# Kernel tuning notes

Hardware: AMD Instinct MI355X
Metric: run time of the kernel (lower is better)

Reference implementation:

```python
import jax, jax.numpy as jnp
import numpy as np

TOPK = 2
NUM_BODY_POINTS = 17
HIDDEN = 64


def bilinear_grid_sample(feat, grid):
    """F.grid_sample(feat, grid, mode='bilinear', padding_mode='zeros', align_corners=False).
    feat: [B,C,H,W]; grid: [B,L,K,2] in [-1,1], grid[...,0]=x (width), grid[...,1]=y (height).
    Returns [B,C,L,K]."""
    B, C, H, W = feat.shape
    x = (grid[..., 0] + 1.0) * (0.5 * W) - 0.5  # [B,L,K]
    y = (grid[..., 1] + 1.0) * (0.5 * H) - 0.5
    x0 = jnp.floor(x)
    y0 = jnp.floor(y)
    wx1 = x - x0
    wy1 = y - y0
    featf = feat.reshape(B, C, H * W)

    def gather(xi, yi):
        valid = (xi >= 0) & (xi < W) & (yi >= 0) & (yi < H)  # [B,L,K]
        xc = jnp.clip(xi, 0, W - 1).astype(jnp.int32)
        yc = jnp.clip(yi, 0, H - 1).astype(jnp.int32)
        idx = (yc * W + xc).reshape(B, -1)  # [B, L*K]
        v = jax.vmap(lambda f, i: f[:, i])(featf, idx)  # [B,C,L*K]
        v = v.reshape(B, C, *xi.shape[1:])  # [B,C,L,K]
        return v * valid[:, None].astype(feat.dtype)

    w00 = ((1 - wx1) * (1 - wy1))[:, None]
    w10 = (wx1 * (1 - wy1))[:, None]
    w01 = ((1 - wx1) * wy1)[:, None]
    w11 = (wx1 * wy1)[:, None]
    return (gather(x0, y0) * w00 + gather(x0 + 1, y0) * w10
            + gather(x0, y0 + 1) * w01 + gather(x0 + 1, y0 + 1) * w11)


def setup_inputs() -> dict:
    key = jax.random.key(0)
    ks = jax.random.split(key, 8)
    B, L, K, C, H, Wd = 16, 1000, NUM_BODY_POINTS, 17, 256, 256
    in_dim = K * (TOPK + 1)
    scores = jax.random.normal(ks[0], (B, L, 1), dtype=jnp.float32)
    pred_poses = jax.random.uniform(ks[1], (B, L, 2 * K), dtype=jnp.float32)
    feat = jax.random.normal(ks[2], (B, C, H, Wd), dtype=jnp.float32)
    s1 = 1.0 / np.sqrt(in_dim)
    s2 = 1.0 / np.sqrt(HIDDEN)
    w1 = jax.random.uniform(ks[3], (HIDDEN, in_dim), minval=-s1, maxval=s1, dtype=jnp.float32)
    b1 = jax.random.uniform(ks[4], (HIDDEN,), minval=-s1, maxval=s1, dtype=jnp.float32)
    w2 = jax.random.uniform(ks[5], (1, HIDDEN), minval=-s2, maxval=s2, dtype=jnp.float32)
    b2 = jax.random.uniform(ks[6], (1,), minval=-s2, maxval=s2, dtype=jnp.float32)
    return {"scores": scores, "pred_poses": pred_poses, "feat": feat,
            "w1": w1, "b1": b1, "w2": w2, "b2": b2}


def reference(scores, pred_poses, feat, w1, b1, w2, b2):
    B, L = pred_poses.shape[:2]
    poses = pred_poses.reshape(B, L, NUM_BODY_POINTS, 2)
    sampled = bilinear_grid_sample(feat, 2.0 * poses - 1.0)  # [B,C,L,K]
    sampled = jnp.transpose(sampled, (0, 2, 3, 1))  # [B,L,K,C]
    prob_topk, _ = jax.lax.top_k(sampled, TOPK)  # [B,L,K,topk]
    stat = jnp.concatenate([prob_topk, prob_topk.mean(axis=-1, keepdims=True)], axis=-1)
    x = stat.reshape(B, L, -1)  # [B,L,K*(topk+1)]
    h = jax.nn.relu(jnp.einsum('bli,hi->blh', x, w1) + b1)
    quality = jnp.einsum('blh,oh->blo', h, w2) + b2  # [B,L,1]
    return scores + quality
```

## Files before the change

kernel.cpp:

```cpp
#include <hip/hip_runtime.h>
#include <hip/hip_bf16.h>
#include <math.h>

#define NB 16
#define NL 1000
#define NK 17
#define NC 17
#define NH 256
#define NW 256
#define HID 64
#define IN_DIM 51
#define NPAIR (NB*NL)
#define PADC 20
#define STATW 52
#define NSAMP (NPAIR*NK)
#define SAMP_PER_XCD (NSAMP/8)
#define BLKS_B 133
#define PPB_C 32
#define PPB_F 15

#define TOP2(v) do { const float _v = (v); \
    if (_v > m1) { m2 = m1; m1 = _v; } else if (_v > m2) { m2 = _v; } } while (0)

__global__ __launch_bounds__(256) void transpose_feat(
    const float* __restrict__ feat, float* __restrict__ featT)
{
    __shared__ float s[NC][257];
    const int bid = blockIdx.x;
    const int l   = ((bid & 7) << 9) | (bid >> 3);
    const int b   = l >> 8;
    const int hw0 = (l & 255) << 8;
    const int tid = threadIdx.x;
    const float* fb = feat + (size_t)b * NC * (NH * NW) + hw0;
    #pragma unroll
    for (int c = 0; c < NC; ++c)
        s[c][tid] = fb[c * (NH * NW) + tid];
    __syncthreads();
    float4* outp = reinterpret_cast<float4*>(
        featT + ((size_t)b * (NH * NW) + hw0) * PADC);
    #pragma unroll
    for (int i = tid; i < 256 * PADC / 4; i += 256) {
        const int p = i / 5;
        const int j = i - 5 * p;
        float4 v;
        if (j < 4) {
            const int c = 4 * j;
            v = make_float4(s[c][p], s[c + 1][p], s[c + 2][p], s[c + 3][p]);
        } else {
            v = make_float4(s[16][p], 0.f, 0.f, 0.f);
        }
        outp[i] = v;
    }
}

__global__ __launch_bounds__(256) void sample_top2(
    const float* __restrict__ pred_poses,
    const float* __restrict__ featT,
    float* __restrict__ stat)
{
    const int xcd = blockIdx.x & 7;
    const int idx = blockIdx.x >> 3;
    const int sl  = idx * 256 + threadIdx.x;
    if (sl >= SAMP_PER_XCD) return;
    const int s    = xcd * SAMP_PER_XCD + sl;
    const int pair = s / NK;
    const int k    = s - pair * NK;
    const int b    = pair / NL;

    const float2 p = *reinterpret_cast<const float2*>(
        pred_poses + (size_t)pair * (2 * NK) + 2 * k);
    const float gx = 2.0f * p.x - 1.0f;
    const float gy = 2.0f * p.y - 1.0f;
    const float fx = (gx + 1.0f) * (0.5f * NW) - 0.5f;
    const float fy = (gy + 1.0f) * (0.5f * NH) - 0.5f;
    const float x0f = floorf(fx), y0f = floorf(fy);
    const float wx = fx - x0f,   wy = fy - y0f;
    const int ix0 = (int)x0f, iy0 = (int)y0f;
    const int ix1 = ix0 + 1,  iy1 = iy0 + 1;
    const float vx0 = (ix0 >= 0 && ix0 < NW) ? 1.f : 0.f;
    const float vx1 = (ix1 >= 0 && ix1 < NW) ? 1.f : 0.f;
    const float vy0 = (iy0 >= 0 && iy0 < NH) ? 1.f : 0.f;
    const float vy1 = (iy1 >= 0 && iy1 < NH) ? 1.f : 0.f;
    const float w00 = (1.f - wx) * (1.f - wy) * vx0 * vy0;
    const float w10 = wx * (1.f - wy) * vx1 * vy0;
    const float w01 = (1.f - wx) * wy * vx0 * vy1;
    const float w11 = wx * wy * vx1 * vy1;
    const int cx0 = min(max(ix0, 0), NW - 1), cx1 = min(max(ix1, 0), NW - 1);
    const int cy0 = min(max(iy0, 0), NH - 1), cy1 = min(max(iy1, 0), NH - 1);
    const float* fb  = featT + (size_t)b * (NH * NW) * PADC;
    const float* p00 = fb + (size_t)(cy0 * NW + cx0) * PADC;
    const float* p10 = fb + (size_t)(cy0 * NW + cx1) * PADC;
    const float* p01 = fb + (size_t)(cy1 * NW + cx0) * PADC;
    const float* p11 = fb + (size_t)(cy1 * NW + cx1) * PADC;

    float m1 = -INFINITY, m2 = -INFINITY;
    #pragma unroll
    for (int j = 0; j < 4; ++j) {
        const float4 a  = *reinterpret_cast<const float4*>(p00 + 4 * j);
        const float4 bq = *reinterpret_cast<const float4*>(p10 + 4 * j);
        const float4 c  = *reinterpret_cast<const float4*>(p01 + 4 * j);
        const float4 d  = *reinterpret_cast<const float4*>(p11 + 4 * j);
        TOP2(w00 * a.x + w10 * bq.x + w01 * c.x + w11 * d.x);
        TOP2(w00 * a.y + w10 * bq.y + w01 * c.y + w11 * d.y);
        TOP2(w00 * a.z + w10 * bq.z + w01 * c.z + w11 * d.z);
        TOP2(w00 * a.w + w10 * bq.w + w01 * c.w + w11 * d.w);
    }
    TOP2(w00 * p00[16] + w10 * p10[16] + w01 * p01[16] + w11 * p11[16]);

    float* sp = stat + (size_t)pair * STATW + 3 * k;
    sp[0] = m1;
    sp[1] = m2;
    sp[2] = 0.5f * (m1 + m2);
}

__global__ __launch_bounds__(256) void mlp_head(
    const float* __restrict__ scores,
    const float* __restrict__ stat,
    const float* __restrict__ w1,
    const float* __restrict__ b1,
    const float* __restrict__ w2,
    const float* __restrict__ b2,
    float* __restrict__ out)
{
    __shared__ float s_w1[HID * IN_DIM];
    __shared__ float s_b1[HID];
    __shared__ float s_w2[HID];
    const int tid = threadIdx.x;
    for (int i = tid; i < HID * IN_DIM; i += 256) s_w1[i] = w1[i];
    if (tid < HID) { s_b1[tid] = b1[tid]; s_w2[tid] = w2[tid]; }
    __syncthreads();

    const int lane = tid & 63;
    const int wv   = tid >> 6;
    float w1r[IN_DIM];
    #pragma unroll
    for (int i = 0; i < IN_DIM; ++i) w1r[i] = s_w1[lane * IN_DIM + i];
    const float hb = s_b1[lane];
    const float hw = s_w2[lane];
    const float vb2 = b2[0];

    const int p0 = blockIdx.x * PPB_C + wv * (PPB_C / 4);
    #pragma unroll
    for (int j = 0; j < PPB_C / 4; ++j) {
        const int pair = p0 + j;
        const float* xp = stat + (size_t)pair * STATW;
        float h = hb;
        #pragma unroll
        for (int i = 0; i < IN_DIM; ++i)
            h = fmaf(xp[i], w1r[i], h);
        h = fmaxf(h, 0.f);
        float pval = h * hw;
        #pragma unroll
        for (int off = 32; off >= 1; off >>= 1)
            pval += __shfl_xor(pval, off, 64);
        if (lane == 0) out[pair] = scores[pair] + pval + vb2;
    }
}

__global__ __launch_bounds__(256) void lqe_fused_direct(
    const float* __restrict__ scores,
    const float* __restrict__ pred_poses,
    const float* __restrict__ feat,
    const float* __restrict__ w1,
    const float* __restrict__ b1,
    const float* __restrict__ w2,
    const float* __restrict__ b2,
    float* __restrict__ out)
{
    __shared__ float s_w1[HID * IN_DIM];
    __shared__ float s_b1[HID];
    __shared__ float s_w2[HID];
    __shared__ float s_x[PPB_F][IN_DIM + 1];

    const int tid = threadIdx.x;
    for (int i = tid; i < HID * IN_DIM; i += 256) s_w1[i] = w1[i];
    if (tid < HID) { s_b1[tid] = b1[tid]; s_w2[tid] = w2[tid]; }

    if (tid < PPB_F * NK) {
        const int lp = tid / NK;
        const int k  = tid - lp * NK;
        const int pair = blockIdx.x * PPB_F + lp;
        if (pair < NPAIR) {
            const int b = pair / NL;
            const float2 p = *reinterpret_cast<const float2*>(
                pred_poses + (size_t)pair * (2 * NK) + 2 * k);
            const float gx = 2.0f * p.x - 1.0f;
            const float gy = 2.0f * p.y - 1.0f;
            const float fx = (gx + 1.0f) * (0.5f * NW) - 0.5f;
            const float fy = (gy + 1.0f) * (0.5f * NH) - 0.5f;
            const float x0f = floorf(fx), y0f = floorf(fy);
            const float wx = fx - x0f,   wy = fy - y0f;
            const int ix0 = (int)x0f, iy0 = (int)y0f;
            const int ix1 = ix0 + 1,  iy1 = iy0 + 1;
            const float vx0 = (ix0 >= 0 && ix0 < NW) ? 1.f : 0.f;
            const float vx1 = (ix1 >= 0 && ix1 < NW) ? 1.f : 0.f;
            const float vy0 = (iy0 >= 0 && iy0 < NH) ? 1.f : 0.f;
            const float vy1 = (iy1 >= 0 && iy1 < NH) ? 1.f : 0.f;
            const float w00 = (1.f - wx) * (1.f - wy) * vx0 * vy0;
            const float w10 = wx * (1.f - wy) * vx1 * vy0;
            const float w01 = (1.f - wx) * wy * vx0 * vy1;
            const float w11 = wx * wy * vx1 * vy1;
            const int cx0 = min(max(ix0, 0), NW - 1), cx1 = min(max(ix1, 0), NW - 1);
            const int cy0 = min(max(iy0, 0), NH - 1), cy1 = min(max(iy1, 0), NH - 1);
            const int o00 = cy0 * NW + cx0, o10 = cy0 * NW + cx1;
            const int o01 = cy1 * NW + cx0, o11 = cy1 * NW + cx1;
            const float* fb = feat + (size_t)b * NC * NH * NW;
            float m1 = -INFINITY, m2 = -INFINITY;
            #pragma unroll
            for (int c = 0; c < NC; ++c) {
                const float* fc = fb + c * (NH * NW);
                TOP2(w00 * fc[o00] + w10 * fc[o10] + w01 * fc[o01] + w11 * fc[o11]);
            }
            s_x[lp][3 * k + 0] = m1;
            s_x[lp][3 * k + 1] = m2;
            s_x[lp][3 * k + 2] = 0.5f * (m1 + m2);
        }
    }
    __syncthreads();

    const int wv = tid >> 6;
    const int lane = tid & 63;
    const float vb2 = b2[0];
    for (int lp = wv; lp < PPB_F; lp += 4) {
        const int pair = blockIdx.x * PPB_F + lp;
        if (pair >= NPAIR) break;
        float h = s_b1[lane];
        #pragma unroll
        for (int i = 0; i < IN_DIM; ++i)
            h = fmaf(s_x[lp][i], s_w1[lane * IN_DIM + i], h);
        h = fmaxf(h, 0.f);
        float pval = h * s_w2[lane];
        #pragma unroll
        for (int off = 32; off >= 1; off >>= 1)
            pval += __shfl_xor(pval, off, 64);
        if (lane == 0) out[pair] = scores[pair] + pval + vb2;
    }
}

extern "C" void kernel_launch(void* const* d_in, const int* in_sizes, int n_in,
                              void* d_out, int out_size, void* d_ws, size_t ws_size,
                              hipStream_t stream) {
    const float* scores     = (const float*)d_in[0];
    const float* pred_poses = (const float*)d_in[1];
    const float* feat       = (const float*)d_in[2];
    const float* w1         = (const float*)d_in[3];
    const float* b1         = (const float*)d_in[4];
    const float* w2         = (const float*)d_in[5];
    const float* b2         = (const float*)d_in[6];
    float* out = (float*)d_out;

    const size_t bytesT = (size_t)NB * NH * NW * PADC * sizeof(float);
    const size_t bytesS = (size_t)NPAIR * STATW * sizeof(float);

    if (ws_size >= bytesT + bytesS) {
        float* featT = (float*)d_ws;
        float* stat  = (float*)((char*)d_ws + bytesT);
        transpose_feat<<<NB * 256, 256, 0, stream>>>(feat, featT);
        sample_top2<<<8 * BLKS_B, 256, 0, stream>>>(pred_poses, featT, stat);
        mlp_head<<<NPAIR / PPB_C, 256, 0, stream>>>(scores, stat,
                                                    w1, b1, w2, b2, out);
    } else {
        const int grid = (NPAIR + PPB_F - 1) / PPB_F;
        lqe_fused_direct<<<grid, 256, 0, stream>>>(scores, pred_poses, feat,
                                                   w1, b1, w2, b2, out);
    }
}
```

Before: 179.2 us.

## Split each bilinear sample across four lanes, one per corner, with shuffle reduction

```diff
diff --git a/kernel.cpp b/kernel.cpp
--- a/kernel.cpp
+++ b/kernel.cpp
@@ -14,10 +14,10 @@
 #define PADC 20
 #define STATW 52
 #define NSAMP (NPAIR*NK)
-#define SAMP_PER_XCD (NSAMP/8)
-#define BLKS_B 133
 #define PPB_C 32
 #define PPB_F 15
+
+typedef float f32x4 __attribute__((ext_vector_type(4)));
 
 #define TOP2(v) do { const float _v = (v); \
     if (_v > m1) { m2 = m1; m1 = _v; } else if (_v > m2) { m2 = _v; } } while (0)
@@ -58,11 +58,9 @@
     const float* __restrict__ featT,
     float* __restrict__ stat)
 {
-    const int xcd = blockIdx.x & 7;
-    const int idx = blockIdx.x >> 3;
-    const int sl  = idx * 256 + threadIdx.x;
-    if (sl >= SAMP_PER_XCD) return;
-    const int s    = xcd * SAMP_PER_XCD + sl;
+    const int t  = blockIdx.x * 256 + threadIdx.x;
+    const int s  = t >> 2;
+    const int cr = t & 3;
     const int pair = s / NK;
     const int k    = s - pair * NK;
     const int b    = pair / NL;
@@ -75,42 +73,53 @@
     const float fy = (gy + 1.0f) * (0.5f * NH) - 0.5f;
     const float x0f = floorf(fx), y0f = floorf(fy);
     const float wx = fx - x0f,   wy = fy - y0f;
-    const int ix0 = (int)x0f, iy0 = (int)y0f;
-    const int ix1 = ix0 + 1,  iy1 = iy0 + 1;
-    const float vx0 = (ix0 >= 0 && ix0 < NW) ? 1.f : 0.f;
-    const float vx1 = (ix1 >= 0 && ix1 < NW) ? 1.f : 0.f;
-    const float vy0 = (iy0 >= 0 && iy0 < NH) ? 1.f : 0.f;
-    const float vy1 = (iy1 >= 0 && iy1 < NH) ? 1.f : 0.f;
-    const float w00 = (1.f - wx) * (1.f - wy) * vx0 * vy0;
-    const float w10 = wx * (1.f - wy) * vx1 * vy0;
-    const float w01 = (1.f - wx) * wy * vx0 * vy1;
-    const float w11 = wx * wy * vx1 * vy1;
-    const int cx0 = min(max(ix0, 0), NW - 1), cx1 = min(max(ix1, 0), NW - 1);
-    const int cy0 = min(max(iy0, 0), NH - 1), cy1 = min(max(iy1, 0), NH - 1);
-    const float* fb  = featT + (size_t)b * (NH * NW) * PADC;
-    const float* p00 = fb + (size_t)(cy0 * NW + cx0) * PADC;
-    const float* p10 = fb + (size_t)(cy0 * NW + cx1) * PADC;
-    const float* p01 = fb + (size_t)(cy1 * NW + cx0) * PADC;
-    const float* p11 = fb + (size_t)(cy1 * NW + cx1) * PADC;
-
+
+    const int dx = cr & 1, dy = cr >> 1;
+    const int ix = (int)x0f + dx;
+    const int iy = (int)y0f + dy;
+    const float fxw = dx ? wx : (1.f - wx);
+    const float fyw = dy ? wy : (1.f - wy);
+    const float vx  = (ix >= 0 && ix < NW) ? 1.f : 0.f;
+    const float vy  = (iy >= 0 && iy < NH) ? 1.f : 0.f;
+    const float wc  = fxw * fyw * vx * vy;
+    const int cx = min(max(ix, 0), NW - 1);
+    const int cy = min(max(iy, 0), NH - 1);
+    const float* rp = featT + ((size_t)b * (NH * NW) + (size_t)(cy * NW + cx)) * PADC;
+
+    const f32x4 r0 = __builtin_nontemporal_load((const f32x4*)(rp));
+    const f32x4 r1 = __builtin_nontemporal_load((const f32x4*)(rp + 4));
+    const f32x4 r2 = __builtin_nontemporal_load((const f32x4*)(rp + 8));
+    const f32x4 r3 = __builtin_nontemporal_load((const f32x4*)(rp + 12));
+    const float r4 = __builtin_nontemporal_load(rp + 16);
+
+    float v[NC];
+    #pragma unroll
+    for (int j = 0; j < 4; ++j) {
+        v[4 * j + 0] = wc * r0[0], v[4 * j + 1] = wc * r0[1],
+        v[4 * j + 2] = wc * r0[2], v[4 * j + 3] = wc * r0[3];
+    }
+    v[0]  = wc * r0[0]; v[1]  = wc * r0[1]; v[2]  = wc * r0[2]; v[3]  = wc * r0[3];
+    v[4]  = wc * r1[0]; v[5]  = wc * r1[1]; v[6]  = wc * r1[2]; v[7]  = wc * r1[3];
+    v[8]  = wc * r2[0]; v[9]  = wc * r2[1]; v[10] = wc * r2[2]; v[11] = wc * r2[3];
+    v[12] = wc * r3[0]; v[13] = wc * r3[1]; v[14] = wc * r3[2]; v[15] = wc * r3[3];
+    v[16] = wc * r4;
+
+    const int lane = threadIdx.x & 63;
+    const int base = lane & ~3;
     float m1 = -INFINITY, m2 = -INFINITY;
     #pragma unroll
-    for (int j = 0; j < 4; ++j) {
-        const float4 a  = *reinterpret_cast<const float4*>(p00 + 4 * j);
-        const float4 bq = *reinterpret_cast<const float4*>(p10 + 4 * j);
-        const float4 c  = *reinterpret_cast<const float4*>(p01 + 4 * j);
-        const float4 d  = *reinterpret_cast<const float4*>(p11 + 4 * j);
-        TOP2(w00 * a.x + w10 * bq.x + w01 * c.x + w11 * d.x);
-        TOP2(w00 * a.y + w10 * bq.y + w01 * c.y + w11 * d.y);
-        TOP2(w00 * a.z + w10 * bq.z + w01 * c.z + w11 * d.z);
-        TOP2(w00 * a.w + w10 * bq.w + w01 * c.w + w11 * d.w);
-    }
-    TOP2(w00 * p00[16] + w10 * p10[16] + w01 * p01[16] + w11 * p11[16]);
-
-    float* sp = stat + (size_t)pair * STATW + 3 * k;
-    sp[0] = m1;
-    sp[1] = m2;
-    sp[2] = 0.5f * (m1 + m2);
+    for (int c = 0; c < NC; ++c) {
+        const float t1 = __shfl(v[c], base + 1, 64);
+        const float t2 = __shfl(v[c], base + 2, 64);
+        const float t3 = __shfl(v[c], base + 3, 64);
+        TOP2(((v[c] + t1) + t2) + t3);
+    }
+    if (cr == 0) {
+        float* sp = stat + (size_t)pair * STATW + 3 * k;
+        sp[0] = m1;
+        sp[1] = m2;
+        sp[2] = 0.5f * (m1 + m2);
+    }
 }
 
 __global__ __launch_bounds__(256) void mlp_head(
@@ -135,8 +144,8 @@
     float w1r[IN_DIM];
     #pragma unroll
     for (int i = 0; i < IN_DIM; ++i) w1r[i] = s_w1[lane * IN_DIM + i];
-    const float hb = s_b1[lane];
-    const float hw = s_w2[lane];
+    const float hb  = s_b1[lane];
+    const float hw  = s_w2[lane];
     const float vb2 = b2[0];
 
     const int p0 = blockIdx.x * PPB_C + wv * (PPB_C / 4);
@@ -256,7 +265,7 @@
         float* featT = (float*)d_ws;
         float* stat  = (float*)((char*)d_ws + bytesT);
         transpose_feat<<<NB * 256, 256, 0, stream>>>(feat, featT);
-        sample_top2<<<8 * BLKS_B, 256, 0, stream>>>(pred_poses, featT, stat);
+        sample_top2<<<(NSAMP * 4) / 256, 256, 0, stream>>>(pred_poses, featT, stat);
         mlp_head<<<NPAIR / PPB_C, 256, 0, stream>>>(scores, stat,
                                                     w1, b1, w2, b2, out);
     } else {
```

Measured after the change: 192.5 us. +7.4%, slower.
